# Optimization experiments

Measured on AMD Instinct MI355X. Metric: run time of the kernel, lower is better.

## Reference

```python
import jax, jax.numpy as jnp
import numpy as np
from jax import lax

D_MODEL = 512
D_STATE = 64
D_CONV = 4
EXPAND = 2
D_INNER = D_MODEL * EXPAND  # 1024
BATCH = 2
SEQ = 2048


def setup_inputs() -> dict:
    key = jax.random.key(0)
    ks = jax.random.split(key, 8)
    s_in = 1.0 / np.sqrt(D_MODEL)
    s_xp = 1.0 / np.sqrt(D_INNER)
    inp = {
        "x": jax.random.normal(ks[0], (BATCH, SEQ, D_MODEL), dtype=jnp.float32),
        "in_proj_w": jax.random.uniform(ks[1], (2 * D_INNER, D_MODEL), minval=-s_in, maxval=s_in),
        "in_proj_b": jnp.zeros((2 * D_INNER,), jnp.float32),
        "conv_w": jax.random.uniform(ks[2], (D_INNER, 1, D_CONV), minval=-0.5, maxval=0.5),
        "conv_b": jnp.zeros((D_INNER,), jnp.float32),
        "x_proj_w": jax.random.uniform(ks[3], (2 * D_STATE + D_INNER, D_INNER), minval=-s_xp, maxval=s_xp),
        "x_proj_b": jnp.zeros((2 * D_STATE + D_INNER,), jnp.float32),
        "A_log": jnp.log(jnp.broadcast_to(jnp.arange(1, D_STATE + 1, dtype=jnp.float32)[None, :], (D_INNER, D_STATE))).copy(),
        "D": jnp.ones((D_INNER,), jnp.float32),
        "out_proj_w": jax.random.uniform(ks[4], (D_MODEL, D_INNER), minval=-s_xp, maxval=s_xp),
        "out_proj_b": jnp.zeros((D_MODEL,), jnp.float32),
    }
    return inp


def _silu(v):
    return v * jax.nn.sigmoid(v)


def reference(x, in_proj_w, in_proj_b, conv_w, conv_b, x_proj_w, x_proj_b,
              A_log, D, out_proj_w, out_proj_b):
    # in_proj: (B,S,Dm) -> (B,S,2*Di)
    x_and_res = x @ in_proj_w.T + in_proj_b
    x_inner, res = jnp.split(x_and_res, [D_INNER], axis=-1)

    # depthwise causal conv1d (torch pads both sides then slices [:S] == left-pad K-1)
    lhs = x_inner.transpose(0, 2, 1)  # (B,Di,S)
    x_conv = lax.conv_general_dilated(
        lhs, conv_w, window_strides=(1,), padding=[(D_CONV - 1, 0)],
        feature_group_count=D_INNER,
        dimension_numbers=("NCH", "OIH", "NCH"))
    x_conv = (x_conv + conv_b[None, :, None]).transpose(0, 2, 1)  # (B,S,Di)
    x_conv = _silu(x_conv)

    # input-dependent SSM params
    ssm = x_conv @ x_proj_w.T + x_proj_b
    Bm, Cm, delta = jnp.split(ssm, [D_STATE, 2 * D_STATE], axis=-1)
    delta = jax.nn.softplus(delta)  # (B,S,Di)

    A = -jnp.exp(A_log)  # (Di,Ds)

    def step(h, inp):
        xt, dt, Bt, Ct = inp  # (B,Di),(B,Di),(B,Ds),(B,Ds)
        dA = jnp.exp(dt[:, :, None] * A)                       # (B,Di,Ds)
        h = dA * h + (dt[:, :, None] * Bt[:, None, :]) * xt[:, :, None]
        yt = jnp.einsum("bds,bs->bd", h, Ct) + D * xt
        return h, yt

    xs = (x_conv.transpose(1, 0, 2), delta.transpose(1, 0, 2),
          Bm.transpose(1, 0, 2), Cm.transpose(1, 0, 2))
    h0 = jnp.zeros((x.shape[0], D_INNER, D_STATE), x.dtype)
    _, ys = lax.scan(step, h0, xs)
    y = ys.transpose(1, 0, 2)  # (B,S,Di)

    y = y * _silu(res)
    return y @ out_proj_w.T + out_proj_b
```

## Files before the change

### kernel.cpp

```cpp
#include <hip/hip_runtime.h>
#include <math.h>

#define DM 512
#define DI 1024
#define DS 64
#define SEQL 2048
#define NB 2
#define NROWS (NB * SEQL)
#define DPROJ (2 * DS + DI)
#define NC 64
#define CL (SEQL / NC)
#define RB 8

typedef unsigned short u16;
typedef __attribute__((ext_vector_type(8))) short bf16x8;
typedef __attribute__((ext_vector_type(4))) float f32x4;

__device__ __forceinline__ u16 f2bf(float f) {
    unsigned u = __builtin_bit_cast(unsigned, f);
    unsigned r = 0x7FFFu + ((u >> 16) & 1u);
    return (u16)((u + r) >> 16);
}
__device__ __forceinline__ float bf2f(u16 u) {
    return __builtin_bit_cast(float, ((unsigned)u) << 16);
}
__device__ __forceinline__ float sel8(const float* a, int k) {
    float lo01 = (k & 1) ? a[1] : a[0];
    float lo23 = (k & 1) ? a[3] : a[2];
    float lo45 = (k & 1) ? a[5] : a[4];
    float lo67 = (k & 1) ? a[7] : a[6];
    float q0 = (k & 2) ? lo23 : lo01;
    float q1 = (k & 2) ? lo67 : lo45;
    return (k & 4) ? q1 : q0;
}

__global__ __launch_bounds__(256) void split_kernel(
    const float* __restrict__ in, u16* __restrict__ hi, u16* __restrict__ lo, int n4)
{
    int i = blockIdx.x * 256 + threadIdx.x;
    if (i >= n4) return;
    float4 v = ((const float4*)in)[i];
    float vv[4] = {v.x, v.y, v.z, v.w};
    unsigned hp[2], lp[2];
    u16 h[4], l[4];
#pragma unroll
    for (int j = 0; j < 4; ++j) {
        h[j] = f2bf(vv[j]);
        l[j] = f2bf(vv[j] - bf2f(h[j]));
    }
    hp[0] = (unsigned)h[0] | ((unsigned)h[1] << 16);
    hp[1] = (unsigned)h[2] | ((unsigned)h[3] << 16);
    lp[0] = (unsigned)l[0] | ((unsigned)l[1] << 16);
    lp[1] = (unsigned)l[2] | ((unsigned)l[3] << 16);
    *(uint2*)(hi + (size_t)i * 4) = make_uint2(hp[0], hp[1]);
    *(uint2*)(lo + (size_t)i * 4) = make_uint2(lp[0], lp[1]);
}

template<int BM, int BN, int MINW>
__global__ __launch_bounds__(256, MINW) void gemm_split(
    const u16* __restrict__ Ah, const u16* __restrict__ Al,
    const u16* __restrict__ Wh, const u16* __restrict__ Wl,
    const float* __restrict__ bias, float* __restrict__ C,
    int M, int N, int K, int spcol)
{
    constexpr int AM = BM / 32;
    constexpr int AN = BN / 32;
    constexpr int SA = BM / 64;
    constexpr int SW = BN / 64;
    __shared__ u16 ldsA[2][2][BM][32];
    __shared__ u16 ldsW[2][2][BN][32];

    const int tid = threadIdx.x;
    const int lane = tid & 63;
    const int w = tid >> 6;
    const int wr = w >> 1, wc = w & 1;

    const int nwg = gridDim.x * gridDim.y;
    const int bid = blockIdx.y * gridDim.x + blockIdx.x;
    const int swz = (bid & 7) * (nwg >> 3) + (bid >> 3);
    const int m0 = (swz / gridDim.x) * BM;
    const int n0 = (swz % gridDim.x) * BN;

    const int srow = lane >> 2;
    const int sc = (((lane & 3) ^ ((srow >> 1) & 3)) << 3);

    f32x4 acc[AM][AN];
#pragma unroll
    for (int m = 0; m < AM; ++m)
#pragma unroll
        for (int n = 0; n < AN; ++n)
            acc[m][n] = (f32x4){0.f, 0.f, 0.f, 0.f};

    const int KT = K >> 5;

    auto stage = [&](int buf, int kt) {
        const int k0 = kt << 5;
#pragma unroll
        for (int s = 0; s < SA; ++s) {
            const int rt = s * 64 + w * 16 + srow;
            const size_t ka = (size_t)(m0 + rt) * K + (k0 + sc);
            __builtin_amdgcn_global_load_lds((const __attribute__((address_space(1))) void*)(Ah + ka),
                (__attribute__((address_space(3))) void*)&ldsA[buf][0][s * 64 + w * 16][0], 16, 0, 0);
            __builtin_amdgcn_global_load_lds((const __attribute__((address_space(1))) void*)(Al + ka),
                (__attribute__((address_space(3))) void*)&ldsA[buf][1][s * 64 + w * 16][0], 16, 0, 0);
        }
#pragma unroll
        for (int s = 0; s < SW; ++s) {
            const int rt = s * 64 + w * 16 + srow;
            const size_t kb = (size_t)(n0 + rt) * K + (k0 + sc);
            __builtin_amdgcn_global_load_lds((const __attribute__((address_space(1))) void*)(Wh + kb),
                (__attribute__((address_space(3))) void*)&ldsW[buf][0][s * 64 + w * 16][0], 16, 0, 0);
            __builtin_amdgcn_global_load_lds((const __attribute__((address_space(1))) void*)(Wl + kb),
                (__attribute__((address_space(3))) void*)&ldsW[buf][1][s * 64 + w * 16][0], 16, 0, 0);
        }
    };

    stage(0, 0);
    int cur = 0;

    const int fr = lane & 15;
    const int chA = ((((lane >> 4)) ^ ((fr >> 1) & 3)) << 3);

    for (int kt = 0; kt < KT; ++kt) {
        __syncthreads();
        if (kt + 1 < KT) stage(cur ^ 1, kt + 1);

        bf16x8 ahf[AM], alf[AM], whf[AN], wlf[AN];
#pragma unroll
        for (int m = 0; m < AM; ++m) {
            const int row = wr * (BM / 2) + m * 16 + fr;
            ahf[m] = *(const bf16x8*)&ldsA[cur][0][row][chA];
            alf[m] = *(const bf16x8*)&ldsA[cur][1][row][chA];
        }
#pragma unroll
        for (int n = 0; n < AN; ++n) {
            const int row = wc * (BN / 2) + n * 16 + fr;
            whf[n] = *(const bf16x8*)&ldsW[cur][0][row][chA];
            wlf[n] = *(const bf16x8*)&ldsW[cur][1][row][chA];
        }
#pragma unroll
        for (int m = 0; m < AM; ++m)
#pragma unroll
            for (int n = 0; n < AN; ++n) {
                acc[m][n] = __builtin_amdgcn_mfma_f32_16x16x32_bf16(ahf[m], whf[n], acc[m][n], 0, 0, 0);
                acc[m][n] = __builtin_amdgcn_mfma_f32_16x16x32_bf16(alf[m], whf[n], acc[m][n], 0, 0, 0);
                acc[m][n] = __builtin_amdgcn_mfma_f32_16x16x32_bf16(ahf[m], wlf[n], acc[m][n], 0, 0, 0);
            }
        cur ^= 1;
    }

    const int r0 = m0 + wr * (BM / 2);
    const int c0 = n0 + wc * (BN / 2) + fr;
    const int rq = (lane >> 4) * 4;
#pragma unroll
    for (int n = 0; n < AN; ++n) {
        const int c = c0 + n * 16;
        const float bs = bias[c];
        const bool sp = (c >= spcol);
#pragma unroll
        for (int m = 0; m < AM; ++m) {
#pragma unroll
            for (int q = 0; q < 4; ++q) {
                const int r = r0 + m * 16 + rq + q;
                float v = acc[m][n][q] + bs;
                if (sp) v = v > 20.f ? v : log1pf(__expf(v));
                C[(size_t)r * N + c] = v;
            }
        }
    }
}

__global__ __launch_bounds__(256) void conv_silu_kernel(
    const float* __restrict__ xz, const float* __restrict__ cw,
    const float* __restrict__ cb,
    u16* __restrict__ xch, u16* __restrict__ xcl)
{
    int idx = blockIdx.x * blockDim.x + threadIdx.x;
    if (idx >= NROWS * DI) return;
    int d = idx & (DI - 1);
    int r = idx >> 10;
    int t = r & (SEQL - 1);
    float acc = cb[d];
#pragma unroll
    for (int k = 0; k < 4; ++k) {
        int tt = t - 3 + k;
        if (tt >= 0)
            acc += cw[d * 4 + k] * xz[(size_t)(r - 3 + k) * (2 * DI) + d];
    }
    float sg = 1.f / (1.f + __expf(-acc));
    float v = acc * sg;
    u16 hi = f2bf(v);
    xch[idx] = hi;
    xcl[idx] = f2bf(v - bf2f(hi));
}


__global__ __launch_bounds__(256) void scan_phase1(
    const float* __restrict__ ssm,
    const u16* __restrict__ xch, const u16* __restrict__ xcl,
    float* __restrict__ Hbuf, float* __restrict__ Sdt)
{
    __shared__ float lb[CL][DS];
    __shared__ float ldtT[32][36];
    __shared__ float lxT[32][36];
    const int tid = threadIdx.x;
    const int sub = tid & 7;
    const int dg = tid >> 3;
    const int gg = blockIdx.x * 32 + dg;
    const int c  = gg >> 11;
    const int ch = gg & (NB * DI - 1);
    const int b = ch >> 10;
    const int d = ch & (DI - 1);
    const int ch0 = (blockIdx.x * 32) & (NB * DI - 1);
    const int d0 = ch0 & (DI - 1);
    const int s0 = sub * 8;
    const float c0 = -(float)(s0 + 1);

    const float* ssmB = ssm + (size_t)b * SEQL * DPROJ;
    const int t0 = c * CL;

#pragma unroll
    for (int i = 0; i < (CL * DS / 4) / 256; ++i) {
        int idx = i * 256 + tid;
        int r = idx >> 4;
        int c4 = (idx & 15) << 2;
        *(float4*)&lb[r][c4] = *(const float4*)(ssmB + (size_t)(t0 + r) * DPROJ + c4);
    }
    {
        int r = tid >> 3;
        int c4 = (tid & 7) << 2;
        float4 v = *(const float4*)(ssmB + (size_t)(t0 + r) * DPROJ + 2 * DS + d0 + c4);
        ldtT[c4 + 0][r] = v.x; ldtT[c4 + 1][r] = v.y;
        ldtT[c4 + 2][r] = v.z; ldtT[c4 + 3][r] = v.w;
    }
    {
        int r = tid >> 3;
        int c4 = (tid & 7) << 2;
        size_t base = ((size_t)(b * SEQL) + t0 + r) * DI + d0 + c4;
        uint2 hh = *(const uint2*)(xch + base);
        uint2 ll = *(const uint2*)(xcl + base);
        lxT[c4 + 0][r] = bf2f((u16)(hh.x)) + bf2f((u16)(ll.x));
        lxT[c4 + 1][r] = bf2f((u16)(hh.x >> 16)) + bf2f((u16)(ll.x >> 16));
        lxT[c4 + 2][r] = bf2f((u16)(hh.y)) + bf2f((u16)(ll.y));
        lxT[c4 + 3][r] = bf2f((u16)(hh.y >> 16)) + bf2f((u16)(ll.y >> 16));
    }
    __syncthreads();

    float h[8] = {0.f,0.f,0.f,0.f,0.f,0.f,0.f,0.f};
    float sdt = 0.f;

    for (int tb = 0; tb < CL; tb += RB) {
        float4 wa = *(const float4*)&ldtT[dg][tb];
        float4 wb = *(const float4*)&ldtT[dg][tb + 4];
        float4 xa = *(const float4*)&lxT[dg][tb];
        float4 xb = *(const float4*)&lxT[dg][tb + 4];
        float dts[8] = {wa.x, wa.y, wa.z, wa.w, wb.x, wb.y, wb.z, wb.w};
        float xv[8]  = {xa.x, xa.y, xa.z, xa.w, xb.x, xb.y, xb.z, xb.w};
#pragma unroll
        for (int j = 0; j < RB; ++j) {
            const int tl = tb + j;
            float4 b0 = *(const float4*)&lb[tl][s0];
            float4 b1 = *(const float4*)&lb[tl][s0 + 4];
            float dt = dts[j];
            float x  = xv[j];
            float dtx = dt * x;
            sdt += dt;
            float q = __expf(-dt);
            float e = __expf(dt * c0);
            h[0] = e * h[0] + dtx * b0.x;  e *= q;
            h[1] = e * h[1] + dtx * b0.y;  e *= q;
            h[2] = e * h[2] + dtx * b0.z;  e *= q;
            h[3] = e * h[3] + dtx * b0.w;  e *= q;
            h[4] = e * h[4] + dtx * b1.x;  e *= q;
            h[5] = e * h[5] + dtx * b1.y;  e *= q;
            h[6] = e * h[6] + dtx * b1.z;  e *= q;
            h[7] = e * h[7] + dtx * b1.w;
        }
    }
    size_t off = ((size_t)(b * DI + d) * NC + c) * DS + s0;
    *(float4*)(Hbuf + off)     = make_float4(h[0], h[1], h[2], h[3]);
    *(float4*)(Hbuf + off + 4) = make_float4(h[4], h[5], h[6], h[7]);
    if (sub == 0) Sdt[(size_t)(b * DI + d) * NC + c] = sdt;
}

__global__ __launch_bounds__(256) void scan_phase2(
    float* __restrict__ Hbuf, const float* __restrict__ Sdt)
{
    int idx = blockIdx.x * 256 + threadIdx.x;
    int bd = idx >> 6;
    int s  = idx & 63;
    float as = -(float)(s + 1);
    size_t base = (size_t)bd * NC * DS + s;
    float hin = 0.f;
#pragma unroll 8
    for (int c = 0; c < NC; ++c) {
        size_t off = base + (size_t)c * DS;
        float he = Hbuf[off];
        float P = __expf(as * Sdt[(size_t)bd * NC + c]);
        Hbuf[off] = hin;
        hin = he + P * hin;
    }
}

__global__ __launch_bounds__(256) void scan_phase3(
    const float* __restrict__ ssm,
    u16* __restrict__ xch, u16* __restrict__ xcl,
    const float* __restrict__ xz,
    const float* __restrict__ dvec, const float* __restrict__ Hbuf)
{
    __shared__ float lbc[CL][2 * DS];
    __shared__ float ldtT[32][36];
    __shared__ float lxT[32][36];
    const int tid = threadIdx.x;
    const int sub = tid & 7;
    const int dg = tid >> 3;
    const int gg = blockIdx.x * 32 + dg;
    const int c  = gg >> 11;
    const int ch = gg & (NB * DI - 1);
    const int b = ch >> 10;
    const int d = ch & (DI - 1);
    const int ch0 = (blockIdx.x * 32) & (NB * DI - 1);
    const int d0 = ch0 & (DI - 1);
    const int s0 = sub * 8;
    const float c0 = -(float)(s0 + 1);

    const float Dv = dvec[d];

    const float* ssmB = ssm + (size_t)b * SEQL * DPROJ;
    u16* xchB = xch + (size_t)b * SEQL * DI;
    u16* xclB = xcl + (size_t)b * SEQL * DI;
    const float* xzB = xz + (size_t)b * SEQL * (2 * DI);
    const int t0 = c * CL;

#pragma unroll
    for (int i = 0; i < (CL * 2 * DS / 4) / 256; ++i) {
        int idx = i * 256 + tid;
        int r = idx >> 5;
        int c4 = (idx & 31) << 2;
        *(float4*)&lbc[r][c4] = *(const float4*)(ssmB + (size_t)(t0 + r) * DPROJ + c4);
    }
    {
        int r = tid >> 3;
        int c4 = (tid & 7) << 2;
        float4 v = *(const float4*)(ssmB + (size_t)(t0 + r) * DPROJ + 2 * DS + d0 + c4);
        ldtT[c4 + 0][r] = v.x; ldtT[c4 + 1][r] = v.y;
        ldtT[c4 + 2][r] = v.z; ldtT[c4 + 3][r] = v.w;
    }
    {
        int r = tid >> 3;
        int c4 = (tid & 7) << 2;
        size_t base = ((size_t)(b * SEQL) + t0 + r) * DI + d0 + c4;
        uint2 hh = *(const uint2*)(xch + base);
        uint2 ll = *(const uint2*)(xcl + base);
        lxT[c4 + 0][r] = bf2f((u16)(hh.x)) + bf2f((u16)(ll.x));
        lxT[c4 + 1][r] = bf2f((u16)(hh.x >> 16)) + bf2f((u16)(ll.x >> 16));
        lxT[c4 + 2][r] = bf2f((u16)(hh.y)) + bf2f((u16)(ll.y));
        lxT[c4 + 3][r] = bf2f((u16)(hh.y >> 16)) + bf2f((u16)(ll.y >> 16));
    }
    __syncthreads();

    float h[8];
    {
        size_t hoff = ((size_t)(b * DI + d) * NC + c) * DS + s0;
        float4 h0 = *(const float4*)(Hbuf + hoff);
        float4 h1 = *(const float4*)(Hbuf + hoff + 4);
        h[0]=h0.x; h[1]=h0.y; h[2]=h0.z; h[3]=h0.w;
        h[4]=h1.x; h[5]=h1.y; h[6]=h1.z; h[7]=h1.w;
    }

    for (int tb = 0; tb < CL; tb += RB) {
        float4 wa = *(const float4*)&ldtT[dg][tb];
        float4 wb = *(const float4*)&ldtT[dg][tb + 4];
        float4 xa = *(const float4*)&lxT[dg][tb];
        float4 xb = *(const float4*)&lxT[dg][tb + 4];
        float dts[8] = {wa.x, wa.y, wa.z, wa.w, wb.x, wb.y, wb.z, wb.w};
        float xv[8]  = {xa.x, xa.y, xa.z, xa.w, xb.x, xb.y, xb.z, xb.w};
        float pv[RB];
#pragma unroll
        for (int j = 0; j < RB; ++j) {
            const int tl = tb + j;
            float4 b0  = *(const float4*)&lbc[tl][s0];
            float4 b1  = *(const float4*)&lbc[tl][s0 + 4];
            float4 cc0 = *(const float4*)&lbc[tl][DS + s0];
            float4 cc1 = *(const float4*)&lbc[tl][DS + s0 + 4];
            float dt = dts[j];
            float x  = xv[j];
            float dtx = dt * x;
            float q = __expf(-dt);
            float e = __expf(dt * c0);
            float pl;
            h[0] = e * h[0] + dtx * b0.x;  pl  = h[0] * cc0.x;  e *= q;
            h[1] = e * h[1] + dtx * b0.y;  pl += h[1] * cc0.y;  e *= q;
            h[2] = e * h[2] + dtx * b0.z;  pl += h[2] * cc0.z;  e *= q;
            h[3] = e * h[3] + dtx * b0.w;  pl += h[3] * cc0.w;  e *= q;
            h[4] = e * h[4] + dtx * b1.x;  pl += h[4] * cc1.x;  e *= q;
            h[5] = e * h[5] + dtx * b1.y;  pl += h[5] * cc1.y;  e *= q;
            h[6] = e * h[6] + dtx * b1.z;  pl += h[6] * cc1.z;  e *= q;
            h[7] = e * h[7] + dtx * b1.w;  pl += h[7] * cc1.w;
            pv[j] = pl;
        }
#pragma unroll
        for (int mm = 1; mm <= 4; mm <<= 1)
#pragma unroll
            for (int j = 0; j < RB; ++j)
                pv[j] += __shfl_xor(pv[j], mm);
        {
            float pvS = sel8(pv, sub);
            float xvS = sel8(xv, sub);
            const int t = t0 + tb + sub;
            float res = xzB[(size_t)t * (2 * DI) + DI + d];
            float sg = res / (1.f + __expf(-res));
            float yv = (pvS + Dv * xvS) * sg;
            u16 hi = f2bf(yv);
            xchB[(size_t)t * DI + d] = hi;
            xclB[(size_t)t * DI + d] = f2bf(yv - bf2f(hi));
        }
    }
}

extern "C" void kernel_launch(void* const* d_in, const int* in_sizes, int n_in,
                              void* d_out, int out_size, void* d_ws, size_t ws_size,
                              hipStream_t stream)
{
    const float* x    = (const float*)d_in[0];
    const float* ipw  = (const float*)d_in[1];
    const float* ipb  = (const float*)d_in[2];
    const float* cw   = (const float*)d_in[3];
    const float* cb   = (const float*)d_in[4];
    const float* xpw  = (const float*)d_in[5];
    const float* xpb  = (const float*)d_in[6];
    const float* dvec = (const float*)d_in[8];
    const float* opw  = (const float*)d_in[9];
    const float* opb  = (const float*)d_in[10];
    float* out = (float*)d_out;

    float* ws = (float*)d_ws;
    float* xz   = ws;
    float* ssm  = xz   + (size_t)NROWS * 2 * DI;
    float* Hbuf = ssm  + (size_t)NROWS * DPROJ;
    float* Sdt  = Hbuf + (size_t)NB * DI * NC * DS;
    u16*   xch  = (u16*)(Sdt + (size_t)NB * DI * NC);
    u16*   xcl  = xch + (size_t)NROWS * DI;
    u16*   wih  = xcl + (size_t)NROWS * DI;
    u16*   wil  = wih + (size_t)2 * DI * DM;
    u16*   wxh  = wil + (size_t)2 * DI * DM;
    u16*   wxl  = wxh + (size_t)DPROJ * DI;
    u16*   woh  = wxl + (size_t)DPROJ * DI;
    u16*   wol  = woh + (size_t)DM * DI;
    u16*   xh   = (u16*)Hbuf;
    u16*   xl   = xh + (size_t)NROWS * DM;

    const int BIG = 1 << 30;

    split_kernel<<<(NROWS * DM / 4) / 256, 256, 0, stream>>>(x, xh, xl, NROWS * DM / 4);
    split_kernel<<<(2 * DI * DM / 4) / 256, 256, 0, stream>>>(ipw, wih, wil, 2 * DI * DM / 4);
    split_kernel<<<(DPROJ * DI / 4) / 256, 256, 0, stream>>>(xpw, wxh, wxl, DPROJ * DI / 4);
    split_kernel<<<(DM * DI / 4) / 256, 256, 0, stream>>>(opw, woh, wol, DM * DI / 4);

    gemm_split<128, 128, 2><<<dim3(2 * DI / 128, NROWS / 128), 256, 0, stream>>>(
        xh, xl, wih, wil, ipb, xz, NROWS, 2 * DI, DM, BIG);
    conv_silu_kernel<<<(NROWS * DI) / 256, 256, 0, stream>>>(xz, cw, cb, xch, xcl);
    gemm_split<128, 64, 3><<<dim3(DPROJ / 64, NROWS / 128), 256, 0, stream>>>(
        xch, xcl, wxh, wxl, xpb, ssm, NROWS, DPROJ, DI, 2 * DS);
    scan_phase1<<<(NB * DI * NC) / 32, 256, 0, stream>>>(ssm, xch, xcl, Hbuf, Sdt);
    scan_phase2<<<(NB * DI * DS) / 256, 256, 0, stream>>>(Hbuf, Sdt);
    scan_phase3<<<(NB * DI * NC) / 32, 256, 0, stream>>>(ssm, xch, xcl, xz, dvec, Hbuf);
    gemm_split<64, 64, 3><<<dim3(DM / 64, NROWS / 64), 256, 0, stream>>>(
        xch, xcl, woh, wol, opb, out, NROWS, DM, DI, BIG);
}
```

Measured before the change: 252.2 us.

## Process two channels per thread in scan phases and use reduce-scatter shuffles

New measurement: 262.1 us. 3.9% more time.

```diff
diff --git a/kernel.cpp b/kernel.cpp
--- a/kernel.cpp
+++ b/kernel.cpp
@@ -33,6 +33,27 @@
     float q1 = (k & 2) ? lo67 : lo45;
     return (k & 4) ? q1 : q0;
 }
+__device__ __forceinline__ float reduce8_to_lane(const float* pv, int sub) {
+    float a0 = (sub & 1) ? pv[1] : pv[0];
+    float o0 = (sub & 1) ? pv[0] : pv[1];
+    float a1 = (sub & 1) ? pv[3] : pv[2];
+    float o1 = (sub & 1) ? pv[2] : pv[3];
+    float a2 = (sub & 1) ? pv[5] : pv[4];
+    float o2 = (sub & 1) ? pv[4] : pv[5];
+    float a3 = (sub & 1) ? pv[7] : pv[6];
+    float o3 = (sub & 1) ? pv[6] : pv[7];
+    a0 += __shfl_xor(o0, 1); a1 += __shfl_xor(o1, 1);
+    a2 += __shfl_xor(o2, 1); a3 += __shfl_xor(o3, 1);
+    float b0 = (sub & 2) ? a1 : a0;
+    float p0 = (sub & 2) ? a0 : a1;
+    float b1 = (sub & 2) ? a3 : a2;
+    float p1 = (sub & 2) ? a2 : a3;
+    b0 += __shfl_xor(p0, 2); b1 += __shfl_xor(p1, 2);
+    float c0 = (sub & 4) ? b1 : b0;
+    float r0 = (sub & 4) ? b0 : b1;
+    c0 += __shfl_xor(r0, 4);
+    return c0;
+}
 
 __global__ __launch_bounds__(256) void split_kernel(
     const float* __restrict__ in, u16* __restrict__ hi, u16* __restrict__ lo, int n4)
@@ -201,41 +222,45 @@
     float* __restrict__ Hbuf, float* __restrict__ Sdt)
 {
     __shared__ float lb[CL][DS];
-    __shared__ float ldtT[32][36];
-    __shared__ float lxT[32][36];
+    __shared__ float ldtT[64][36];
+    __shared__ float lxT[64][36];
     const int tid = threadIdx.x;
     const int sub = tid & 7;
     const int dg = tid >> 3;
-    const int gg = blockIdx.x * 32 + dg;
-    const int c  = gg >> 11;
-    const int ch = gg & (NB * DI - 1);
-    const int b = ch >> 10;
-    const int d = ch & (DI - 1);
-    const int ch0 = (blockIdx.x * 32) & (NB * DI - 1);
+    const int bid = blockIdx.x;
+    const int c  = bid >> 5;
+    const int ch0 = (bid & 31) * 64;
+    const int b = ch0 >> 10;
     const int d0 = ch0 & (DI - 1);
+    const int d_a = d0 + dg;
+    const int d_b = d_a + 32;
     const int s0 = sub * 8;
-    const float c0 = -(float)(s0 + 1);
+    const float a0c = -(float)(s0 + 1);
 
     const float* ssmB = ssm + (size_t)b * SEQL * DPROJ;
     const int t0 = c * CL;
 
 #pragma unroll
-    for (int i = 0; i < (CL * DS / 4) / 256; ++i) {
+    for (int i = 0; i < 2; ++i) {
         int idx = i * 256 + tid;
         int r = idx >> 4;
         int c4 = (idx & 15) << 2;
         *(float4*)&lb[r][c4] = *(const float4*)(ssmB + (size_t)(t0 + r) * DPROJ + c4);
     }
-    {
-        int r = tid >> 3;
-        int c4 = (tid & 7) << 2;
+#pragma unroll
+    for (int i = 0; i < 2; ++i) {
+        int idx = i * 256 + tid;
+        int r = idx >> 4;
+        int c4 = (idx & 15) << 2;
         float4 v = *(const float4*)(ssmB + (size_t)(t0 + r) * DPROJ + 2 * DS + d0 + c4);
         ldtT[c4 + 0][r] = v.x; ldtT[c4 + 1][r] = v.y;
         ldtT[c4 + 2][r] = v.z; ldtT[c4 + 3][r] = v.w;
     }
-    {
-        int r = tid >> 3;
-        int c4 = (tid & 7) << 2;
+#pragma unroll
+    for (int i = 0; i < 2; ++i) {
+        int idx = i * 256 + tid;
+        int r = idx >> 4;
+        int c4 = (idx & 15) << 2;
         size_t base = ((size_t)(b * SEQL) + t0 + r) * DI + d0 + c4;
         uint2 hh = *(const uint2*)(xch + base);
         uint2 ll = *(const uint2*)(xcl + base);
@@ -246,41 +271,71 @@
     }
     __syncthreads();
 
-    float h[8] = {0.f,0.f,0.f,0.f,0.f,0.f,0.f,0.f};
-    float sdt = 0.f;
+    float h[16];
+#pragma unroll
+    for (int i = 0; i < 16; ++i) h[i] = 0.f;
+    float sdt_a = 0.f, sdt_b = 0.f;
 
     for (int tb = 0; tb < CL; tb += RB) {
         float4 wa = *(const float4*)&ldtT[dg][tb];
         float4 wb = *(const float4*)&ldtT[dg][tb + 4];
+        float4 va = *(const float4*)&ldtT[dg + 32][tb];
+        float4 vb = *(const float4*)&ldtT[dg + 32][tb + 4];
         float4 xa = *(const float4*)&lxT[dg][tb];
         float4 xb = *(const float4*)&lxT[dg][tb + 4];
-        float dts[8] = {wa.x, wa.y, wa.z, wa.w, wb.x, wb.y, wb.z, wb.w};
-        float xv[8]  = {xa.x, xa.y, xa.z, xa.w, xb.x, xb.y, xb.z, xb.w};
+        float4 ya = *(const float4*)&lxT[dg + 32][tb];
+        float4 yb = *(const float4*)&lxT[dg + 32][tb + 4];
+        float dA[8] = {wa.x, wa.y, wa.z, wa.w, wb.x, wb.y, wb.z, wb.w};
+        float dB[8] = {va.x, va.y, va.z, va.w, vb.x, vb.y, vb.z, vb.w};
+        float xA[8] = {xa.x, xa.y, xa.z, xa.w, xb.x, xb.y, xb.z, xb.w};
+        float xB[8] = {ya.x, ya.y, ya.z, ya.w, yb.x, yb.y, yb.z, yb.w};
 #pragma unroll
         for (int j = 0; j < RB; ++j) {
             const int tl = tb + j;
             float4 b0 = *(const float4*)&lb[tl][s0];
             float4 b1 = *(const float4*)&lb[tl][s0 + 4];
-            float dt = dts[j];
-            float x  = xv[j];
-            float dtx = dt * x;
-            sdt += dt;
-            float q = __expf(-dt);
-            float e = __expf(dt * c0);
-            h[0] = e * h[0] + dtx * b0.x;  e *= q;
-            h[1] = e * h[1] + dtx * b0.y;  e *= q;
-            h[2] = e * h[2] + dtx * b0.z;  e *= q;
-            h[3] = e * h[3] + dtx * b0.w;  e *= q;
-            h[4] = e * h[4] + dtx * b1.x;  e *= q;
-            h[5] = e * h[5] + dtx * b1.y;  e *= q;
-            h[6] = e * h[6] + dtx * b1.z;  e *= q;
-            h[7] = e * h[7] + dtx * b1.w;
-        }
-    }
-    size_t off = ((size_t)(b * DI + d) * NC + c) * DS + s0;
-    *(float4*)(Hbuf + off)     = make_float4(h[0], h[1], h[2], h[3]);
-    *(float4*)(Hbuf + off + 4) = make_float4(h[4], h[5], h[6], h[7]);
-    if (sub == 0) Sdt[(size_t)(b * DI + d) * NC + c] = sdt;
+            {
+                float dt = dA[j], x = xA[j];
+                float dtx = dt * x;
+                sdt_a += dt;
+                float q = __expf(-dt);
+                float e = __expf(dt * a0c);
+                h[0] = e * h[0] + dtx * b0.x;  e *= q;
+                h[1] = e * h[1] + dtx * b0.y;  e *= q;
+                h[2] = e * h[2] + dtx * b0.z;  e *= q;
+                h[3] = e * h[3] + dtx * b0.w;  e *= q;
+                h[4] = e * h[4] + dtx * b1.x;  e *= q;
+                h[5] = e * h[5] + dtx * b1.y;  e *= q;
+                h[6] = e * h[6] + dtx * b1.z;  e *= q;
+                h[7] = e * h[7] + dtx * b1.w;
+            }
+            {
+                float dt = dB[j], x = xB[j];
+                float dtx = dt * x;
+                sdt_b += dt;
+                float q = __expf(-dt);
+                float e = __expf(dt * a0c);
+                h[8]  = e * h[8]  + dtx * b0.x;  e *= q;
+                h[9]  = e * h[9]  + dtx * b0.y;  e *= q;
+                h[10] = e * h[10] + dtx * b0.z;  e *= q;
+                h[11] = e * h[11] + dtx * b0.w;  e *= q;
+                h[12] = e * h[12] + dtx * b1.x;  e *= q;
+                h[13] = e * h[13] + dtx * b1.y;  e *= q;
+                h[14] = e * h[14] + dtx * b1.z;  e *= q;
+                h[15] = e * h[15] + dtx * b1.w;
+            }
+        }
+    }
+    size_t offA = ((size_t)(b * DI + d_a) * NC + c) * DS + s0;
+    size_t offB = ((size_t)(b * DI + d_b) * NC + c) * DS + s0;
+    *(float4*)(Hbuf + offA)     = make_float4(h[0], h[1], h[2], h[3]);
+    *(float4*)(Hbuf + offA + 4) = make_float4(h[4], h[5], h[6], h[7]);
+    *(float4*)(Hbuf + offB)     = make_float4(h[8], h[9], h[10], h[11]);
+    *(float4*)(Hbuf + offB + 4) = make_float4(h[12], h[13], h[14], h[15]);
+    if (sub == 0) {
+        Sdt[(size_t)(b * DI + d_a) * NC + c] = sdt_a;
+        Sdt[(size_t)(b * DI + d_b) * NC + c] = sdt_b;
+    }
 }
 
 __global__ __launch_bounds__(256) void scan_phase2(
@@ -309,22 +364,23 @@
     const float* __restrict__ dvec, const float* __restrict__ Hbuf)
 {
     __shared__ float lbc[CL][2 * DS];
-    __shared__ float ldtT[32][36];
-    __shared__ float lxT[32][36];
+    __shared__ float ldtT[64][36];
+    __shared__ float lxT[64][36];
     const int tid = threadIdx.x;
     const int sub = tid & 7;
     const int dg = tid >> 3;
-    const int gg = blockIdx.x * 32 + dg;
-    const int c  = gg >> 11;
-    const int ch = gg & (NB * DI - 1);
-    const int b = ch >> 10;
-    const int d = ch & (DI - 1);
-    const int ch0 = (blockIdx.x * 32) & (NB * DI - 1);
+    const int bid = blockIdx.x;
+    const int c  = bid >> 5;
+    const int ch0 = (bid & 31) * 64;
+    const int b = ch0 >> 10;
     const int d0 = ch0 & (DI - 1);
+    const int d_a = d0 + dg;
+    const int d_b = d_a + 32;
     const int s0 = sub * 8;
-    const float c0 = -(float)(s0 + 1);
-
-    const float Dv = dvec[d];
+    const float a0c = -(float)(s0 + 1);
+
+    const float Dv_a = dvec[d_a];
+    const float Dv_b = dvec[d_b];
 
     const float* ssmB = ssm + (size_t)b * SEQL * DPROJ;
     u16* xchB = xch + (size_t)b * SEQL * DI;
@@ -333,22 +389,26 @@
     const int t0 = c * CL;
 
 #pragma unroll
-    for (int i = 0; i < (CL * 2 * DS / 4) / 256; ++i) {
+    for (int i = 0; i < 4; ++i) {
         int idx = i * 256 + tid;
         int r = idx >> 5;
         int c4 = (idx & 31) << 2;
         *(float4*)&lbc[r][c4] = *(const float4*)(ssmB + (size_t)(t0 + r) * DPROJ + c4);
     }
-    {
-        int r = tid >> 3;
-        int c4 = (tid & 7) << 2;
+#pragma unroll
+    for (int i = 0; i < 2; ++i) {
+        int idx = i * 256 + tid;
+        int r = idx >> 4;
+        int c4 = (idx & 15) << 2;
         float4 v = *(const float4*)(ssmB + (size_t)(t0 + r) * DPROJ + 2 * DS + d0 + c4);
         ldtT[c4 + 0][r] = v.x; ldtT[c4 + 1][r] = v.y;
         ldtT[c4 + 2][r] = v.z; ldtT[c4 + 3][r] = v.w;
     }
-    {
-        int r = tid >> 3;
-        int c4 = (tid & 7) << 2;
+#pragma unroll
+    for (int i = 0; i < 2; ++i) {
+        int idx = i * 256 + tid;
+        int r = idx >> 4;
+        int c4 = (idx & 15) << 2;
         size_t base = ((size_t)(b * SEQL) + t0 + r) * DI + d0 + c4;
         uint2 hh = *(const uint2*)(xch + base);
         uint2 ll = *(const uint2*)(xcl + base);
@@ -359,23 +419,34 @@
     }
     __syncthreads();
 
-    float h[8];
+    float h[16];
     {
-        size_t hoff = ((size_t)(b * DI + d) * NC + c) * DS + s0;
-        float4 h0 = *(const float4*)(Hbuf + hoff);
-        float4 h1 = *(const float4*)(Hbuf + hoff + 4);
+        size_t offA = ((size_t)(b * DI + d_a) * NC + c) * DS + s0;
+        size_t offB = ((size_t)(b * DI + d_b) * NC + c) * DS + s0;
+        float4 h0 = *(const float4*)(Hbuf + offA);
+        float4 h1 = *(const float4*)(Hbuf + offA + 4);
+        float4 h2 = *(const float4*)(Hbuf + offB);
+        float4 h3 = *(const float4*)(Hbuf + offB + 4);
         h[0]=h0.x; h[1]=h0.y; h[2]=h0.z; h[3]=h0.w;
         h[4]=h1.x; h[5]=h1.y; h[6]=h1.z; h[7]=h1.w;
+        h[8]=h2.x; h[9]=h2.y; h[10]=h2.z; h[11]=h2.w;
+        h[12]=h3.x; h[13]=h3.y; h[14]=h3.z; h[15]=h3.w;
     }
 
     for (int tb = 0; tb < CL; tb += RB) {
         float4 wa = *(const float4*)&ldtT[dg][tb];
         float4 wb = *(const float4*)&ldtT[dg][tb + 4];
+        float4 va = *(const float4*)&ldtT[dg + 32][tb];
+        float4 vb = *(const float4*)&ldtT[dg + 32][tb + 4];
         float4 xa = *(const float4*)&lxT[dg][tb];
         float4 xb = *(const float4*)&lxT[dg][tb + 4];
-        float dts[8] = {wa.x, wa.y, wa.z, wa.w, wb.x, wb.y, wb.z, wb.w};
-        float xv[8]  = {xa.x, xa.y, xa.z, xa.w, xb.x, xb.y, xb.z, xb.w};
-        float pv[RB];
+        float4 ya = *(const float4*)&lxT[dg + 32][tb];
+        float4 yb = *(const float4*)&lxT[dg + 32][tb + 4];
+        float dA[8] = {wa.x, wa.y, wa.z, wa.w, wb.x, wb.y, wb.z, wb.w};
+        float dB[8] = {va.x, va.y, va.z, va.w, vb.x, vb.y, vb.z, vb.w};
+        float xA[8] = {xa.x, xa.y, xa.z, xa.w, xb.x, xb.y, xb.z, xb.w};
+        float xB[8] = {ya.x, ya.y, ya.z, ya.w, yb.x, yb.y, yb.z, yb.w};
+        float pvA[RB], pvB[RB];
 #pragma unroll
         for (int j = 0; j < RB; ++j) {
             const int tl = tb + j;
@@ -383,37 +454,59 @@
             float4 b1  = *(const float4*)&lbc[tl][s0 + 4];
             float4 cc0 = *(const float4*)&lbc[tl][DS + s0];
             float4 cc1 = *(const float4*)&lbc[tl][DS + s0 + 4];
-            float dt = dts[j];
-            float x  = xv[j];
-            float dtx = dt * x;
-            float q = __expf(-dt);
-            float e = __expf(dt * c0);
-            float pl;
-            h[0] = e * h[0] + dtx * b0.x;  pl  = h[0] * cc0.x;  e *= q;
-            h[1] = e * h[1] + dtx * b0.y;  pl += h[1] * cc0.y;  e *= q;
-            h[2] = e * h[2] + dtx * b0.z;  pl += h[2] * cc0.z;  e *= q;
-            h[3] = e * h[3] + dtx * b0.w;  pl += h[3] * cc0.w;  e *= q;
-            h[4] = e * h[4] + dtx * b1.x;  pl += h[4] * cc1.x;  e *= q;
-            h[5] = e * h[5] + dtx * b1.y;  pl += h[5] * cc1.y;  e *= q;
-            h[6] = e * h[6] + dtx * b1.z;  pl += h[6] * cc1.z;  e *= q;
-            h[7] = e * h[7] + dtx * b1.w;  pl += h[7] * cc1.w;
-            pv[j] = pl;
-        }
-#pragma unroll
-        for (int mm = 1; mm <= 4; mm <<= 1)
-#pragma unroll
-            for (int j = 0; j < RB; ++j)
-                pv[j] += __shfl_xor(pv[j], mm);
+            {
+                float dt = dA[j], x = xA[j];
+                float dtx = dt * x;
+                float q = __expf(-dt);
+                float e = __expf(dt * a0c);
+                float pl;
+                h[0] = e * h[0] + dtx * b0.x;  pl  = h[0] * cc0.x;  e *= q;
+                h[1] = e * h[1] + dtx * b0.y;  pl += h[1] * cc0.y;  e *= q;
+                h[2] = e * h[2] + dtx * b0.z;  pl += h[2] * cc0.z;  e *= q;
+                h[3] = e * h[3] + dtx * b0.w;  pl += h[3] * cc0.w;  e *= q;
+                h[4] = e * h[4] + dtx * b1.x;  pl += h[4] * cc1.x;  e *= q;
+                h[5] = e * h[5] + dtx * b1.y;  pl += h[5] * cc1.y;  e *= q;
+                h[6] = e * h[6] + dtx * b1.z;  pl += h[6] * cc1.z;  e *= q;
+                h[7] = e * h[7] + dtx * b1.w;  pl += h[7] * cc1.w;
+                pvA[j] = pl;
+            }
+            {
+                float dt = dB[j], x = xB[j];
+                float dtx = dt * x;
+                float q = __expf(-dt);
+                float e = __expf(dt * a0c);
+                float pl;
+                h[8]  = e * h[8]  + dtx * b0.x;  pl  = h[8]  * cc0.x;  e *= q;
+                h[9]  = e * h[9]  + dtx * b0.y;  pl += h[9]  * cc0.y;  e *= q;
+                h[10] = e * h[10] + dtx * b0.z;  pl += h[10] * cc0.z;  e *= q;
+                h[11] = e * h[11] + dtx * b0.w;  pl += h[11] * cc0.w;  e *= q;
+                h[12] = e * h[12] + dtx * b1.x;  pl += h[12] * cc1.x;  e *= q;
+                h[13] = e * h[13] + dtx * b1.y;  pl += h[13] * cc1.y;  e *= q;
+                h[14] = e * h[14] + dtx * b1.z;  pl += h[14] * cc1.z;  e *= q;
+                h[15] = e * h[15] + dtx * b1.w;  pl += h[15] * cc1.w;
+                pvB[j] = pl;
+            }
+        }
+        float rA = reduce8_to_lane(pvA, sub);
+        float rB = reduce8_to_lane(pvB, sub);
+        float xAs = sel8(xA, sub);
+        float xBs = sel8(xB, sub);
+        const int t = t0 + tb + sub;
         {
-            float pvS = sel8(pv, sub);
-            float xvS = sel8(xv, sub);
-            const int t = t0 + tb + sub;
-            float res = xzB[(size_t)t * (2 * DI) + DI + d];
+            float res = xzB[(size_t)t * (2 * DI) + DI + d_a];
             float sg = res / (1.f + __expf(-res));
-            float yv = (pvS + Dv * xvS) * sg;
+            float yv = (rA + Dv_a * xAs) * sg;
             u16 hi = f2bf(yv);
-            xchB[(size_t)t * DI + d] = hi;
-            xclB[(size_t)t * DI + d] = f2bf(yv - bf2f(hi));
+            xchB[(size_t)t * DI + d_a] = hi;
+            xclB[(size_t)t * DI + d_a] = f2bf(yv - bf2f(hi));
+        }
+        {
+            float res = xzB[(size_t)t * (2 * DI) + DI + d_b];
+            float sg = res / (1.f + __expf(-res));
+            float yv = (rB + Dv_b * xBs) * sg;
+            u16 hi = f2bf(yv);
+            xchB[(size_t)t * DI + d_b] = hi;
+            xclB[(size_t)t * DI + d_b] = f2bf(yv - bf2f(hi));
         }
     }
 }
@@ -462,9 +555,9 @@
     conv_silu_kernel<<<(NROWS * DI) / 256, 256, 0, stream>>>(xz, cw, cb, xch, xcl);
     gemm_split<128, 64, 3><<<dim3(DPROJ / 64, NROWS / 128), 256, 0, stream>>>(
         xch, xcl, wxh, wxl, xpb, ssm, NROWS, DPROJ, DI, 2 * DS);
-    scan_phase1<<<(NB * DI * NC) / 32, 256, 0, stream>>>(ssm, xch, xcl, Hbuf, Sdt);
+    scan_phase1<<<(NB * DI * NC) / 64, 256, 0, stream>>>(ssm, xch, xcl, Hbuf, Sdt);
     scan_phase2<<<(NB * DI * DS) / 256, 256, 0, stream>>>(Hbuf, Sdt);
-    scan_phase3<<<(NB * DI * NC) / 32, 256, 0, stream>>>(ssm, xch, xcl, xz, dvec, Hbuf);
+    scan_phase3<<<(NB * DI * NC) / 64, 256, 0, stream>>>(ssm, xch, xcl, xz, dvec, Hbuf);
     gemm_split<64, 64, 3><<<dim3(DM / 64, NROWS / 64), 256, 0, stream>>>(
         xch, xcl, woh, wol, opb, out, NROWS, DM, DI, BIG);
 }
```
